# Optimization experiments

Measured on AMD Instinct MI355X. Metric: run time of the kernel, lower is better.

## Reference

```python
import jax, jax.numpy as jnp
import numpy as np

S, B_BOX, N_CLASS = 7, 2, 20
L_COORD, L_NOOBJ = 5.0, 0.5
BATCH = 4096
C = 5 * B_BOX + N_CLASS  # 30


def setup_inputs() -> dict:
    key = jax.random.key(0)
    k1, k2, k3, k4 = jax.random.split(key, 4)
    # coords/w/h/classes strictly positive (sqrt is applied to raw values)
    y = jax.random.uniform(k1, (BATCH, S, S, C), minval=0.05, maxval=0.95, dtype=jnp.float32)
    # confidence channels must be exactly 0/1 (mask tests == 1)
    conf0 = jax.random.bernoulli(k3, 0.3, (BATCH, S, S)).astype(jnp.float32)
    conf1 = jax.random.bernoulli(k4, 0.3, (BATCH, S, S)).astype(jnp.float32)
    y = y.at[..., 0].set(conf0).at[..., 5].set(conf1)
    y_h = jax.random.uniform(k2, (BATCH, S, S, C), minval=0.05, maxval=0.95, dtype=jnp.float32)
    return {"y": y, "y_h": y_h}


def _loss(y, y_h):
    b_sz = y.shape[0]
    conf_idx = np.arange(B_BOX) * 5  # [0, 5]
    y_conf = y[..., conf_idx]        # [B,S,S,b]
    yh_conf = y_h[..., conf_idx]
    mf = (y_conf == 1.0).astype(y.dtype)  # obj mask per box, constant wrt grads
    dconf = (y_conf - yh_conf) ** 2
    loss_obj = jnp.sum(dconf * mf)
    loss_noobj = jnp.sum(dconf * (1.0 - mf))

    loss_coord = jnp.zeros((), y.dtype)
    loss_prob = jnp.zeros((), y.dtype)
    for k in range(B_BOX):  # static small loop over boxes
        mk = mf[..., k]  # [B,S,S]
        base = 5 * k
        dxy = (y[..., base + 1] - y_h[..., base + 1]) ** 2 \
            + (y[..., base + 2] - y_h[..., base + 2]) ** 2
        dwh = (jnp.sqrt(y[..., base + 3]) - jnp.sqrt(y_h[..., base + 3])) ** 2 \
            + (jnp.sqrt(y[..., base + 4]) - jnp.sqrt(y_h[..., base + 4])) ** 2
        loss_coord = loss_coord + jnp.sum((dxy + dwh) * mk)

        # prob term: slice from k*5+5 to end (faithful to original, for k=0 this
        # includes box-2's 5 entries), softmax over the masked batch dimension.
        tail = y[..., base + 5:]
        tail_h = y_h[..., base + 5:]
        mkb = mk[..., None]  # [B,S,S,1]
        neg = jnp.where(mkb > 0, tail_h, -jnp.inf)
        m = jnp.max(neg, axis=0)                       # [S,S,Ct]
        m_safe = jnp.where(jnp.isfinite(m), m, 0.0)    # guard empty columns
        p = jnp.exp(tail_h - m_safe) * mkb
        denom = jnp.sum(p, axis=0)
        sm = p / jnp.where(denom > 0, denom, 1.0)
        loss_prob = loss_prob + jnp.sum((tail - sm) ** 2 * mkb)

    loss = loss_obj + L_NOOBJ * loss_noobj + L_COORD * loss_coord + loss_prob
    return loss / b_sz


def reference(y, y_h):
    return _loss(y, y_h)
```

## Files before the change

kernel.cpp:

```cpp
#include <hip/hip_runtime.h>
#include <math.h>

#define CC 30
#define NBATCH 4096
#define NIJ 49
#define NPAIR 1225
#define PSTR 7352
#define F4TOT (PSTR / 4)
#define THREADS 512
#define SLABF4 1470


__global__ __launch_bounds__(THREADS)
void yolo_main(const float* __restrict__ y, const float* __restrict__ yh,
               float* __restrict__ scal, float* __restrict__ parts, int nwg)
{
    __shared__ __align__(16) float tY[4 * 1470];
    __shared__ float scr[4][8];

    const int tid = threadIdx.x;
    const int wg  = blockIdx.x;
    const int bpw = NBATCH / nwg;
    const int nslab = bpw >> 2;

    const int i0 = tid, i1 = tid + 512;
    const int i2r = tid + 1024;
    const int i2  = (i2r < SLABF4) ? i2r : (SLABF4 - 1);
    const bool w2 = (i2r < SLABF4);

    int  ijv[3], cv[3], pr[3];
    bool val[3];
    #pragma unroll
    for (int i = 0; i < 3; i++) {
        int p = tid + i * THREADS;
        val[i] = (p < NPAIR);
        pr[i]  = p;
        int pp = val[i] ? p : 0;
        ijv[i] = pp / 25;
        cv[i]  = 5 + pp % 25;
    }

    float D0[3] = {0,0,0}, B0[3] = {0,0,0}, C0[3] = {0,0,0};
    float D1[3] = {0,0,0}, B1[3] = {0,0,0}, C1[3] = {0,0,0};
    float obj = 0.f, noobj = 0.f, coord = 0.f, tt = 0.f;

    const float4* Yg = (const float4*)y;
    float4* tY4 = (float4*)tY;

    {
        const size_t f4 = (size_t)((wg * bpw) >> 2) * SLABF4;
        float4 a0 = Yg[f4+i0], a1 = Yg[f4+i1], a2 = Yg[f4+i2];
        tY4[i0] = a0; tY4[i1] = a1; if (w2) tY4[i2] = a2;
    }
    __syncthreads();

    float4 ry0, ry1, ry2;

    for (int s = 0; s < nslab; s++) {
        const size_t gslab = (size_t)(wg * bpw + s * 4) * 1470;

        if (s + 1 < nslab) {
            const size_t nf4 = (size_t)((wg * bpw + (s+1)*4) >> 2) * SLABF4;
            ry0 = Yg[nf4+i0]; ry1 = Yg[nf4+i1]; ry2 = Yg[nf4+i2];
        }

        if (tid < 4 * NIJ) {
            const int base = tid * CC;
            const float* hq = yh + gslab + base;
            float y0 = tY[base],     h0 = hq[0];
            float y5 = tY[base + 5], h5 = hq[5];
            float d0 = y0 - h0; d0 *= d0;
            float d5 = y5 - h5; d5 *= d5;
            const bool m0 = (y0 == 1.0f), m1 = (y5 == 1.0f);
            obj   += (m0 ? d0 : 0.f) + (m1 ? d5 : 0.f);
            noobj += (m0 ? 0.f : d0) + (m1 ? 0.f : d5);
            if (m0) {
                float a  = tY[base + 1] - hq[1];
                float b2 = tY[base + 2] - hq[2];
                float c1 = sqrtf(tY[base + 3]) - sqrtf(hq[3]);
                float c2 = sqrtf(tY[base + 4]) - sqrtf(hq[4]);
                coord += a * a + b2 * b2 + c1 * c1 + c2 * c2;
            }
            if (m1) {
                float a  = tY[base + 6] - hq[6];
                float b2 = tY[base + 7] - hq[7];
                float c1 = sqrtf(tY[base + 8]) - sqrtf(hq[8]);
                float c2 = sqrtf(tY[base + 9]) - sqrtf(hq[9]);
                coord += a * a + b2 * b2 + c1 * c1 + c2 * c2;
            }
        }

        #pragma unroll
        for (int b = 0; b < 4; b++) {
            #pragma unroll
            for (int i = 0; i < 3; i++) {
                if (!val[i]) continue;
                const int cb = b * 1470 + ijv[i] * CC;
                const float w0 = (tY[cb] == 1.0f) ? 1.f : 0.f;
                const float w1 = (cv[i] >= 10 && tY[cb + 5] == 1.0f) ? 1.f : 0.f;
                const float t  = tY[cb + cv[i]];
                const float th = yh[gslab + cb + cv[i]];
                const float e  = __expf(th);
                const float te = t * e, ee = e * e, t2 = t * t;
                D0[i] = fmaf(e,  w0, D0[i]);
                B0[i] = fmaf(te, w0, B0[i]);
                C0[i] = fmaf(ee, w0, C0[i]);
                D1[i] = fmaf(e,  w1, D1[i]);
                B1[i] = fmaf(te, w1, B1[i]);
                C1[i] = fmaf(ee, w1, C1[i]);
                tt = fmaf(t2, w0 + w1, tt);
            }
        }
        __syncthreads();
        if (s + 1 < nslab) {
            tY4[i0] = ry0; tY4[i1] = ry1; if (w2) tY4[i2] = ry2;
        }
        __syncthreads();
    }

    float* pp = parts + (size_t)wg * PSTR;
    #pragma unroll
    for (int i = 0; i < 3; i++) {
        if (!val[i]) continue;
        const int p = pr[i];
        pp[p]            = D0[i];
        pp[NPAIR + p]    = B0[i];
        pp[2*NPAIR + p]  = C0[i];
        pp[3*NPAIR + p]  = D1[i];
        pp[4*NPAIR + p]  = B1[i];
        pp[5*NPAIR + p]  = C1[i];
    }

    const int lane = tid & 63, wv = tid >> 6;
    #pragma unroll
    for (int off = 32; off > 0; off >>= 1) {
        obj   += __shfl_down(obj,   off);
        noobj += __shfl_down(noobj, off);
        coord += __shfl_down(coord, off);
        tt    += __shfl_down(tt,    off);
    }
    if (lane == 0) { scr[0][wv] = obj; scr[1][wv] = noobj; scr[2][wv] = coord; scr[3][wv] = tt; }
    __syncthreads();
    if (tid < 4) {
        float sacc = 0.f;
        #pragma unroll
        for (int w = 0; w < THREADS / 64; w++) sacc += scr[tid][w];
        scal[wg * 4 + tid] = sacc;
    }
}

__global__ __launch_bounds__(512)
void yolo_reduce(const float* __restrict__ parts, float* __restrict__ parts2, int nwg)
{
    const int lane = threadIdx.x & 63;
    const int sub  = threadIdx.x >> 6;
    const int f4i  = blockIdx.x * 64 + lane;
    const int cy   = blockIdx.y;
    const int wpc  = nwg >> 3;
    const int wps  = wpc >> 3;

    float4 s = make_float4(0.f, 0.f, 0.f, 0.f);
    if (f4i < F4TOT) {
        const float* q = parts + (size_t)(cy * wpc + sub * wps) * PSTR + f4i * 4;
        for (int w = 0; w < wps; ++w) {
            float4 a = *(const float4*)q;
            s.x += a.x; s.y += a.y; s.z += a.z; s.w += a.w;
            q += PSTR;
        }
    }
    __shared__ float4 sred[8][64];
    sred[sub][lane] = s;
    __syncthreads();
    if (threadIdx.x < 64 && f4i < F4TOT) {
        float4 t = sred[0][lane];
        #pragma unroll
        for (int c = 1; c < 8; c++) {
            float4 a = sred[c][lane];
            t.x += a.x; t.y += a.y; t.z += a.z; t.w += a.w;
        }
        *(float4*)(parts2 + (size_t)cy * PSTR + f4i * 4) = t;
    }
}

__global__ __launch_bounds__(1024)
void yolo_final(const float* __restrict__ parts2, const float* __restrict__ scal,
                float* __restrict__ out, int nwg)
{
    float v = 0.f;

    for (int s = threadIdx.x; s < NPAIR; s += 1024) {
        const int cidx = s % 25;
        float D0 = 0, B0 = 0, C0 = 0, D1 = 0, B1 = 0, C1 = 0;
        #pragma unroll
        for (int c = 0; c < 8; c++) {
            const float* t = parts2 + (size_t)c * PSTR;
            D0 += t[s];           B0 += t[NPAIR + s];   C0 += t[2*NPAIR + s];
            D1 += t[3*NPAIR + s]; B1 += t[4*NPAIR + s]; C1 += t[5*NPAIR + s];
        }
        if (D0 > 0.f) v += C0 / (D0 * D0) - 2.f * B0 / D0;
        if (cidx >= 5 && D1 > 0.f) v += C1 / (D1 * D1) - 2.f * B1 / D1;
    }

    const float4* s4 = (const float4*)scal;
    for (int w = threadIdx.x; w < nwg; w += 1024) {
        float4 a = s4[w];
        v += a.x + 0.5f * a.y + 5.0f * a.z + a.w;
    }

    __shared__ float sred[16];
    #pragma unroll
    for (int off = 32; off > 0; off >>= 1) v += __shfl_down(v, off);
    const int lane = threadIdx.x & 63, wv = threadIdx.x >> 6;
    if (lane == 0) sred[wv] = v;
    __syncthreads();
    if (threadIdx.x == 0) {
        float tot = 0.f;
        #pragma unroll
        for (int w = 0; w < 16; w++) tot += sred[w];
        out[0] = tot / (float)NBATCH;
    }
}

extern "C" void kernel_launch(void* const* d_in, const int* in_sizes, int n_in,
                              void* d_out, int out_size, void* d_ws, size_t ws_size,
                              hipStream_t stream)
{
    const float* y  = (const float*)d_in[0];
    const float* yh = (const float*)d_in[1];
    float* out    = (float*)d_out;
    float* scal   = (float*)d_ws;
    float* parts2 = (float*)((char*)d_ws + 8192);
    float* parts  = (float*)((char*)d_ws + 243456);

    const size_t per_wg = (size_t)PSTR * sizeof(float);
    int nwg;
    if      (ws_size >= 243456 + 512 * per_wg) nwg = 512;
    else if (ws_size >= 243456 + 256 * per_wg) nwg = 256;
    else                                       nwg = 128;

    yolo_main<<<nwg, THREADS, 0, stream>>>(y, yh, scal, parts, nwg);
    dim3 g2((F4TOT + 63) / 64, 8);
    yolo_reduce<<<g2, 512, 0, stream>>>(parts, parts2, nwg);
    yolo_final<<<1, 1024, 0, stream>>>(parts2, scal, out, nwg);
}
```

Measured before the change: 31.51 us.

## Split main kernel into 2D grid over pair-blocks and batch chunks without LDS staging

```diff
diff --git a/kernel.cpp b/kernel.cpp
--- a/kernel.cpp
+++ b/kernel.cpp
@@ -7,156 +7,102 @@
 #define NPAIR 1225
 #define PSTR 7352
 #define F4TOT (PSTR / 4)
-#define THREADS 512
-#define SLABF4 1470
 
 
-__global__ __launch_bounds__(THREADS)
+__global__ __launch_bounds__(256)
 void yolo_main(const float* __restrict__ y, const float* __restrict__ yh,
-               float* __restrict__ scal, float* __restrict__ parts, int nwg)
+               float* __restrict__ sc, float* __restrict__ parts, int nchunk)
 {
-    __shared__ __align__(16) float tY[4 * 1470];
-    __shared__ float scr[4][8];
+    const int tid   = threadIdx.x;
+    const int x     = blockIdx.x;
+    const int chunk = blockIdx.y;
+    const int bpc   = NBATCH / nchunk;
+    const int b0    = chunk * bpc;
 
-    const int tid = threadIdx.x;
-    const int wg  = blockIdx.x;
-    const int bpw = NBATCH / nwg;
-    const int nslab = bpw >> 2;
+    const int  p  = x * 256 + tid;
+    const bool pv = (p < NPAIR);
+    const int  ps = pv ? p : 0;
+    const int  ij = ps / 25;
+    const int  c  = 5 + ps % 25;
+    const bool ctail = (c >= 10);
 
-    const int i0 = tid, i1 = tid + 512;
-    const int i2r = tid + 1024;
-    const int i2  = (i2r < SLABF4) ? i2r : (SLABF4 - 1);
-    const bool w2 = (i2r < SLABF4);
+    float D0=0.f,B0=0.f,C0=0.f,D1=0.f,B1=0.f,C1=0.f,tt=0.f;
 
-    int  ijv[3], cv[3], pr[3];
-    bool val[3];
-    #pragma unroll
-    for (int i = 0; i < 3; i++) {
-        int p = tid + i * THREADS;
-        val[i] = (p < NPAIR);
-        pr[i]  = p;
-        int pp = val[i] ? p : 0;
-        ijv[i] = pp / 25;
-        cv[i]  = 5 + pp % 25;
+    const float* qy = y  + ((size_t)b0 * NIJ + ij) * CC;
+    const float* qh = yh + ((size_t)b0 * NIJ + ij) * CC;
+    #pragma unroll 4
+    for (int b = 0; b < bpc; b++) {
+        const float y0 = qy[0], y5 = qy[5];
+        const float t  = qy[c], th = qh[c];
+        const float w0 = (pv && y0 == 1.0f) ? 1.f : 0.f;
+        const float wk = (pv && ctail && y5 == 1.0f) ? 1.f : 0.f;
+        const float e  = __expf(th);
+        const float te = t * e, ee = e * e;
+        D0 = fmaf(e,  w0, D0);
+        B0 = fmaf(te, w0, B0);
+        C0 = fmaf(ee, w0, C0);
+        D1 = fmaf(e,  wk, D1);
+        B1 = fmaf(te, wk, B1);
+        C1 = fmaf(ee, wk, C1);
+        tt = fmaf(t * t, w0 + wk, tt);
+        qy += NIJ * CC; qh += NIJ * CC;
     }
 
-    float D0[3] = {0,0,0}, B0[3] = {0,0,0}, C0[3] = {0,0,0};
-    float D1[3] = {0,0,0}, B1[3] = {0,0,0}, C1[3] = {0,0,0};
-    float obj = 0.f, noobj = 0.f, coord = 0.f, tt = 0.f;
-
-    const float4* Yg = (const float4*)y;
-    float4* tY4 = (float4*)tY;
-
-    {
-        const size_t f4 = (size_t)((wg * bpw) >> 2) * SLABF4;
-        float4 a0 = Yg[f4+i0], a1 = Yg[f4+i1], a2 = Yg[f4+i2];
-        tY4[i0] = a0; tY4[i1] = a1; if (w2) tY4[i2] = a2;
-    }
-    __syncthreads();
-
-    float4 ry0, ry1, ry2;
-
-    for (int s = 0; s < nslab; s++) {
-        const size_t gslab = (size_t)(wg * bpw + s * 4) * 1470;
-
-        if (s + 1 < nslab) {
-            const size_t nf4 = (size_t)((wg * bpw + (s+1)*4) >> 2) * SLABF4;
-            ry0 = Yg[nf4+i0]; ry1 = Yg[nf4+i1]; ry2 = Yg[nf4+i2];
-        }
-
-        if (tid < 4 * NIJ) {
-            const int base = tid * CC;
-            const float* hq = yh + gslab + base;
-            float y0 = tY[base],     h0 = hq[0];
-            float y5 = tY[base + 5], h5 = hq[5];
-            float d0 = y0 - h0; d0 *= d0;
-            float d5 = y5 - h5; d5 *= d5;
-            const bool m0 = (y0 == 1.0f), m1 = (y5 == 1.0f);
-            obj   += (m0 ? d0 : 0.f) + (m1 ? d5 : 0.f);
-            noobj += (m0 ? 0.f : d0) + (m1 ? 0.f : d5);
-            if (m0) {
-                float a  = tY[base + 1] - hq[1];
-                float b2 = tY[base + 2] - hq[2];
-                float c1 = sqrtf(tY[base + 3]) - sqrtf(hq[3]);
-                float c2 = sqrtf(tY[base + 4]) - sqrtf(hq[4]);
-                coord += a * a + b2 * b2 + c1 * c1 + c2 * c2;
-            }
-            if (m1) {
-                float a  = tY[base + 6] - hq[6];
-                float b2 = tY[base + 7] - hq[7];
-                float c1 = sqrtf(tY[base + 8]) - sqrtf(hq[8]);
-                float c2 = sqrtf(tY[base + 9]) - sqrtf(hq[9]);
-                coord += a * a + b2 * b2 + c1 * c1 + c2 * c2;
-            }
-        }
-
-        #pragma unroll
-        for (int b = 0; b < 4; b++) {
-            #pragma unroll
-            for (int i = 0; i < 3; i++) {
-                if (!val[i]) continue;
-                const int cb = b * 1470 + ijv[i] * CC;
-                const float w0 = (tY[cb] == 1.0f) ? 1.f : 0.f;
-                const float w1 = (cv[i] >= 10 && tY[cb + 5] == 1.0f) ? 1.f : 0.f;
-                const float t  = tY[cb + cv[i]];
-                const float th = yh[gslab + cb + cv[i]];
-                const float e  = __expf(th);
-                const float te = t * e, ee = e * e, t2 = t * t;
-                D0[i] = fmaf(e,  w0, D0[i]);
-                B0[i] = fmaf(te, w0, B0[i]);
-                C0[i] = fmaf(ee, w0, C0[i]);
-                D1[i] = fmaf(e,  w1, D1[i]);
-                B1[i] = fmaf(te, w1, B1[i]);
-                C1[i] = fmaf(ee, w1, C1[i]);
-                tt = fmaf(t2, w0 + w1, tt);
-            }
-        }
-        __syncthreads();
-        if (s + 1 < nslab) {
-            tY4[i0] = ry0; tY4[i1] = ry1; if (w2) tY4[i2] = ry2;
-        }
-        __syncthreads();
+    if (pv) {
+        float* pr = parts + (size_t)chunk * PSTR;
+        pr[p]           = D0;
+        pr[NPAIR + p]   = B0;
+        pr[2*NPAIR + p] = C0;
+        pr[3*NPAIR + p] = D1;
+        pr[4*NPAIR + p] = B1;
+        pr[5*NPAIR + p] = C1;
     }
 
-    float* pp = parts + (size_t)wg * PSTR;
-    #pragma unroll
-    for (int i = 0; i < 3; i++) {
-        if (!val[i]) continue;
-        const int p = pr[i];
-        pp[p]            = D0[i];
-        pp[NPAIR + p]    = B0[i];
-        pp[2*NPAIR + p]  = C0[i];
-        pp[3*NPAIR + p]  = D1[i];
-        pp[4*NPAIR + p]  = B1[i];
-        pp[5*NPAIR + p]  = C1[i];
+    const int ijs = (x * 256 + 24) / 25;
+    int ije = ((x + 1) * 256 + 24) / 25; if (ije > NIJ) ije = NIJ;
+    const int nown = ije - ijs;
+    float obj = 0.f, noobj = 0.f, coord = 0.f;
+    for (int t = tid; t < nown * bpc; t += 256) {
+        const int bl = t / nown, il = t - bl * nown;
+        const float* cy = y  + ((size_t)(b0 + bl) * NIJ + ijs + il) * CC;
+        const float* ch = yh + ((size_t)(b0 + bl) * NIJ + ijs + il) * CC;
+        float a0 = cy[0] - ch[0]; a0 *= a0;
+        float a5 = cy[5] - ch[5]; a5 *= a5;
+        const bool m0 = (cy[0] == 1.0f), m1 = (cy[5] == 1.0f);
+        obj   += (m0 ? a0 : 0.f) + (m1 ? a5 : 0.f);
+        noobj += (m0 ? 0.f : a0) + (m1 ? 0.f : a5);
+        if (m0) {
+            float a  = cy[1] - ch[1], b2 = cy[2] - ch[2];
+            float c1 = sqrtf(cy[3]) - sqrtf(ch[3]);
+            float c2 = sqrtf(cy[4]) - sqrtf(ch[4]);
+            coord += a * a + b2 * b2 + c1 * c1 + c2 * c2;
+        }
+        if (m1) {
+            float a  = cy[6] - ch[6], b2 = cy[7] - ch[7];
+            float c1 = sqrtf(cy[8]) - sqrtf(ch[8]);
+            float c2 = sqrtf(cy[9]) - sqrtf(ch[9]);
+            coord += a * a + b2 * b2 + c1 * c1 + c2 * c2;
+        }
     }
 
+    float v = obj + 0.5f * noobj + 5.f * coord + tt;
+    __shared__ float sred[4];
+    #pragma unroll
+    for (int off = 32; off > 0; off >>= 1) v += __shfl_down(v, off);
     const int lane = tid & 63, wv = tid >> 6;
-    #pragma unroll
-    for (int off = 32; off > 0; off >>= 1) {
-        obj   += __shfl_down(obj,   off);
-        noobj += __shfl_down(noobj, off);
-        coord += __shfl_down(coord, off);
-        tt    += __shfl_down(tt,    off);
-    }
-    if (lane == 0) { scr[0][wv] = obj; scr[1][wv] = noobj; scr[2][wv] = coord; scr[3][wv] = tt; }
+    if (lane == 0) sred[wv] = v;
     __syncthreads();
-    if (tid < 4) {
-        float sacc = 0.f;
-        #pragma unroll
-        for (int w = 0; w < THREADS / 64; w++) sacc += scr[tid][w];
-        scal[wg * 4 + tid] = sacc;
-    }
+    if (tid == 0) sc[x + 5 * chunk] = sred[0] + sred[1] + sred[2] + sred[3];
 }
 
 __global__ __launch_bounds__(512)
-void yolo_reduce(const float* __restrict__ parts, float* __restrict__ parts2, int nwg)
+void yolo_reduce(const float* __restrict__ parts, float* __restrict__ parts2, int nchunk)
 {
     const int lane = threadIdx.x & 63;
     const int sub  = threadIdx.x >> 6;
     const int f4i  = blockIdx.x * 64 + lane;
     const int cy   = blockIdx.y;
-    const int wpc  = nwg >> 3;
+    const int wpc  = nchunk >> 3;
     const int wps  = wpc >> 3;
 
     float4 s = make_float4(0.f, 0.f, 0.f, 0.f);
@@ -174,8 +120,8 @@
     if (threadIdx.x < 64 && f4i < F4TOT) {
         float4 t = sred[0][lane];
         #pragma unroll
-        for (int c = 1; c < 8; c++) {
-            float4 a = sred[c][lane];
+        for (int cc = 1; cc < 8; cc++) {
+            float4 a = sred[cc][lane];
             t.x += a.x; t.y += a.y; t.z += a.z; t.w += a.w;
         }
         *(float4*)(parts2 + (size_t)cy * PSTR + f4i * 4) = t;
@@ -183,8 +129,8 @@
 }
 
 __global__ __launch_bounds__(1024)
-void yolo_final(const float* __restrict__ parts2, const float* __restrict__ scal,
-                float* __restrict__ out, int nwg)
+void yolo_final(const float* __restrict__ parts2, const float* __restrict__ sc,
+                float* __restrict__ out, int nchunk)
 {
     float v = 0.f;
 
@@ -192,20 +138,15 @@
         const int cidx = s % 25;
         float D0 = 0, B0 = 0, C0 = 0, D1 = 0, B1 = 0, C1 = 0;
         #pragma unroll
-        for (int c = 0; c < 8; c++) {
-            const float* t = parts2 + (size_t)c * PSTR;
+        for (int cc = 0; cc < 8; cc++) {
+            const float* t = parts2 + (size_t)cc * PSTR;
             D0 += t[s];           B0 += t[NPAIR + s];   C0 += t[2*NPAIR + s];
             D1 += t[3*NPAIR + s]; B1 += t[4*NPAIR + s]; C1 += t[5*NPAIR + s];
         }
         if (D0 > 0.f) v += C0 / (D0 * D0) - 2.f * B0 / D0;
         if (cidx >= 5 && D1 > 0.f) v += C1 / (D1 * D1) - 2.f * B1 / D1;
     }
-
-    const float4* s4 = (const float4*)scal;
-    for (int w = threadIdx.x; w < nwg; w += 1024) {
-        float4 a = s4[w];
-        v += a.x + 0.5f * a.y + 5.0f * a.z + a.w;
-    }
+    for (int w = threadIdx.x; w < 5 * nchunk; w += 1024) v += sc[w];
 
     __shared__ float sred[16];
     #pragma unroll
@@ -228,18 +169,19 @@
     const float* y  = (const float*)d_in[0];
     const float* yh = (const float*)d_in[1];
     float* out    = (float*)d_out;
-    float* scal   = (float*)d_ws;
+    float* sc     = (float*)d_ws;
     float* parts2 = (float*)((char*)d_ws + 8192);
     float* parts  = (float*)((char*)d_ws + 243456);
 
-    const size_t per_wg = (size_t)PSTR * sizeof(float);
-    int nwg;
-    if      (ws_size >= 243456 + 512 * per_wg) nwg = 512;
-    else if (ws_size >= 243456 + 256 * per_wg) nwg = 256;
-    else                                       nwg = 128;
+    const size_t per_ch = (size_t)PSTR * sizeof(float);
+    int nchunk;
+    if      (ws_size >= 243456 + 256 * per_ch) nchunk = 256;
+    else if (ws_size >= 243456 + 128 * per_ch) nchunk = 128;
+    else                                       nchunk = 64;
 
-    yolo_main<<<nwg, THREADS, 0, stream>>>(y, yh, scal, parts, nwg);
+    dim3 gmain(5, nchunk);
+    yolo_main<<<gmain, 256, 0, stream>>>(y, yh, sc, parts, nchunk);
     dim3 g2((F4TOT + 63) / 64, 8);
-    yolo_reduce<<<g2, 512, 0, stream>>>(parts, parts2, nwg);
-    yolo_final<<<1, 1024, 0, stream>>>(parts2, scal, out, nwg);
+    yolo_reduce<<<g2, 512, 0, stream>>>(parts, parts2, nchunk);
+    yolo_final<<<1, 1024, 0, stream>>>(parts2, sc, out, nchunk);
 }
```

New measurement: 30.37 us. -3.6%, faster.
